# Kernel optimization log

Measured on AMD Instinct MI355X. Metric: run time of the kernel, lower is better.

## Reference

```python
import jax, jax.numpy as jnp
import numpy as np

B = 256        # graphs in batch
N_PER = 512    # nodes per graph (uniform)
D = 256        # in_dim
DEG = 16       # avg degree
RATIO = 0.5


def setup_inputs() -> dict:
    key = jax.random.key(0)
    k1, k2, k3, k4 = jax.random.split(key, 4)
    N = B * N_PER
    e_per = N_PER * DEG
    x = jax.random.normal(k1, (N, D), dtype=jnp.float32)
    # edges confined within each graph (DGL batched-graph structure)
    src = jax.random.randint(k2, (B, e_per), 0, N_PER)
    dst = jax.random.randint(k3, (B, e_per), 0, N_PER)
    offs = jnp.arange(B, dtype=jnp.int32)[:, None] * N_PER
    src = (src + offs).reshape(-1).astype(jnp.int32)
    dst = (dst + offs).reshape(-1).astype(jnp.int32)
    W = jax.random.normal(k4, (D, 1), dtype=jnp.float32) / np.sqrt(D)
    b = jnp.zeros((1,), dtype=jnp.float32)
    num_nodes = jnp.full((B,), N_PER, dtype=jnp.int32)
    return {"x": x, "W": W, "b": b, "src": src, "dst": dst, "num_nodes": num_nodes}


def reference(x, W, b, src, dst, num_nodes):
    N, d = x.shape
    bsz = num_nodes.shape[0]
    n = N // bsz                     # uniform nodes per graph -> static
    k = int(np.ceil(RATIO * n))      # nodes kept per graph (static)

    # ---- GraphConv(in_dim, 1), DGL default norm='both':
    # score = D_in^{-1/2} A D_out^{-1/2} (x W) + b   (W applied first: out_dim < in_dim)
    ones_e = jnp.ones(src.shape, dtype=x.dtype)
    deg_out = jax.ops.segment_sum(ones_e, src, num_segments=N)
    deg_in = jax.ops.segment_sum(ones_e, dst, num_segments=N)
    h = x @ W                                              # [N, 1]
    h = h * jax.lax.rsqrt(jnp.clip(deg_out, 1.0))[:, None]
    agg = jax.ops.segment_sum(h[src], dst, num_segments=N) # [N, 1]
    score = (agg * jax.lax.rsqrt(jnp.clip(deg_in, 1.0))[:, None] + b)[:, 0]  # [N]

    # ---- topk per graph: dense [B, n] buffer is just a reshape (uniform graphs),
    # sort descending + take first k  ==  lax.top_k
    dense = score.reshape(bsz, n)
    _, idx = jax.lax.top_k(dense, k)                       # [B, k] descending
    perm = (idx + jnp.arange(bsz)[:, None] * n).reshape(-1)  # global node ids [B*k]

    # ---- gather + scale: feature[perm] * tanh(score[perm])
    feat = x[perm] * jnp.tanh(score[perm])[:, None]        # [B*k, D]

    # ---- node_subgraph: edges whose both endpoints survive
    keep = jnp.zeros((N,), dtype=bool).at[perm].set(True)
    edge_mask = keep[src] & keep[dst]                      # [E]
    next_num_nodes = jnp.full((bsz,), k, dtype=jnp.int32)
    return feat, perm, edge_mask, next_num_nodes
```

## Files before the change

### kernel.cpp

```cpp
#include <hip/hip_runtime.h>
#include <math.h>

#define BB    256
#define NPER  512
#define DD    256
#define KK    256
#define EPG   (NPER * 16)
#define NN    (BB * NPER)
#define EE    (BB * EPG)

__global__ __launch_bounds__(256) void k_dot(const float* __restrict__ x,
                                             const float* __restrict__ W,
                                             float* __restrict__ hraw) {
    const int wave = threadIdx.x >> 6;
    const int lane = threadIdx.x & 63;
    const int r0   = blockIdx.x * 16 + wave * 4;
    const float4 wv = ((const float4*)W)[lane];
    const float4* p = (const float4*)(x + ((size_t)r0 << 8));
    float4 a0 = p[lane];
    float4 a1 = p[64 + lane];
    float4 a2 = p[128 + lane];
    float4 a3 = p[192 + lane];
    float d0 = a0.x * wv.x + a0.y * wv.y + a0.z * wv.z + a0.w * wv.w;
    float d1 = a1.x * wv.x + a1.y * wv.y + a1.z * wv.z + a1.w * wv.w;
    float d2 = a2.x * wv.x + a2.y * wv.y + a2.z * wv.z + a2.w * wv.w;
    float d3 = a3.x * wv.x + a3.y * wv.y + a3.z * wv.z + a3.w * wv.w;
    #pragma unroll
    for (int off = 32; off > 0; off >>= 1) {
        d0 += __shfl_down(d0, off, 64);
        d1 += __shfl_down(d1, off, 64);
        d2 += __shfl_down(d2, off, 64);
        d3 += __shfl_down(d3, off, 64);
    }
    if (lane == 0) {
        hraw[r0]     = d0;
        hraw[r0 + 1] = d1;
        hraw[r0 + 2] = d2;
        hraw[r0 + 3] = d3;
    }
}

__global__ __launch_bounds__(1024) void k_graph(
        const float* __restrict__ hraw, const float* __restrict__ b,
        const int* __restrict__ src, const int* __restrict__ dst,
        int* __restrict__ perm_i, float* __restrict__ tscore,
        float* __restrict__ out_perm, float* __restrict__ emask,
        float* __restrict__ nnn) {
    __shared__ unsigned short esrc[EPG];
    __shared__ unsigned short edst[EPG];
    __shared__ int   degs[NPER];
    __shared__ int   degd[NPER];
    __shared__ float hl[NPER];
    __shared__ float aggl[NPER];
    __shared__ float scl[NPER];
    __shared__ unsigned long long keys[NPER];
    __shared__ int   keep[NPER];

    const int g = blockIdx.x;
    const int t = threadIdx.x;
    const int nbase = g << 9;

    float hv = 0.0f;
    if (t < NPER) hv = hraw[nbase + t];

    if (t < NPER) { degs[t] = 0; degd[t] = 0; aggl[t] = 0.0f; keep[t] = 0; }
    __syncthreads();

    const int4* s4 = (const int4*)(src + (size_t)g * EPG);
    const int4* d4 = (const int4*)(dst + (size_t)g * EPG);
    unsigned int* es2 = (unsigned int*)esrc;
    unsigned int* ed2 = (unsigned int*)edst;
    #pragma unroll
    for (int i = t; i < EPG / 4; i += 1024) {
        int4 sv = s4[i], dv = d4[i];
        unsigned int s0 = (unsigned int)(sv.x - nbase);
        unsigned int s1 = (unsigned int)(sv.y - nbase);
        unsigned int s2 = (unsigned int)(sv.z - nbase);
        unsigned int s3 = (unsigned int)(sv.w - nbase);
        es2[i * 2]     = s0 | (s1 << 16);
        es2[i * 2 + 1] = s2 | (s3 << 16);
        atomicAdd(&degs[s0], 1); atomicAdd(&degs[s1], 1);
        atomicAdd(&degs[s2], 1); atomicAdd(&degs[s3], 1);
        unsigned int t0 = (unsigned int)(dv.x - nbase);
        unsigned int t1 = (unsigned int)(dv.y - nbase);
        unsigned int t2 = (unsigned int)(dv.z - nbase);
        unsigned int t3 = (unsigned int)(dv.w - nbase);
        ed2[i * 2]     = t0 | (t1 << 16);
        ed2[i * 2 + 1] = t2 | (t3 << 16);
        atomicAdd(&degd[t0], 1); atomicAdd(&degd[t1], 1);
        atomicAdd(&degd[t2], 1); atomicAdd(&degd[t3], 1);
    }
    __syncthreads();

    if (t < NPER) hl[t] = hv * rsqrtf(fmaxf((float)degs[t], 1.0f));
    __syncthreads();

    #pragma unroll
    for (int e = t; e < EPG; e += 1024)
        atomicAdd(&aggl[edst[e]], hl[esrc[e]]);
    __syncthreads();

    if (t < NPER) {
        float sc = aggl[t] * rsqrtf(fmaxf((float)degd[t], 1.0f)) + b[0];
        scl[t] = sc;
        unsigned int u = __float_as_uint(sc);
        u = (u & 0x80000000u) ? ~u : (u | 0x80000000u);
        keys[t] = ((unsigned long long)u << 32) |
                  (unsigned long long)(0xFFFFFFFFu - (unsigned)t);
    }
    __syncthreads();

    for (int kk = 2; kk <= NPER; kk <<= 1) {
        for (int j = kk >> 1; j > 0; j >>= 1) {
            if (t < NPER) {
                int i = t, ixj = t ^ j;
                if (ixj > i) {
                    unsigned long long a = keys[i], c = keys[ixj];
                    bool up = ((i & kk) == 0);
                    if (up ? (a < c) : (a > c)) { keys[i] = c; keys[ixj] = a; }
                }
            }
            __syncthreads();
        }
    }

    if (t < KK) {
        unsigned long long kv = keys[t];
        int idx = (int)(0xFFFFFFFFu - (unsigned int)(kv & 0xFFFFFFFFull));
        int r = (g << 8) + t;
        perm_i[r]   = nbase + idx;
        out_perm[r] = (float)(nbase + idx);
        tscore[r]   = tanhf(scl[idx]);
        keep[idx]   = 1;
    }
    __syncthreads();

    float4* em4 = (float4*)(emask + ((size_t)g << 13));
    #pragma unroll
    for (int i = t; i < EPG / 4; i += 1024) {
        int e = i * 4;
        float4 m;
        m.x = (keep[esrc[e]]     & keep[edst[e]])     ? 1.0f : 0.0f;
        m.y = (keep[esrc[e + 1]] & keep[edst[e + 1]]) ? 1.0f : 0.0f;
        m.z = (keep[esrc[e + 2]] & keep[edst[e + 2]]) ? 1.0f : 0.0f;
        m.w = (keep[esrc[e + 3]] & keep[edst[e + 3]]) ? 1.0f : 0.0f;
        em4[i] = m;
    }
    if (g == 0 && t < BB) nnn[t] = (float)KK;
}

__global__ __launch_bounds__(256) void k_feat(
        const float* __restrict__ x,
        const int* __restrict__ perm_i, const float* __restrict__ tscore,
        float* __restrict__ feat) {
    const int wave = threadIdx.x >> 6;
    const int lane = threadIdx.x & 63;
    const int r = blockIdx.x * 4 + wave;
    const int gid = perm_i[r];
    const float ts = tscore[r];
    float4 v = ((const float4*)(x + ((size_t)gid << 8)))[lane];
    float4 o = make_float4(v.x * ts, v.y * ts, v.z * ts, v.w * ts);
    ((float4*)(feat + ((size_t)r << 8)))[lane] = o;
}

extern "C" void kernel_launch(void* const* d_in, const int* in_sizes, int n_in,
                              void* d_out, int out_size, void* d_ws, size_t ws_size,
                              hipStream_t stream) {
    const float* x   = (const float*)d_in[0];
    const float* W   = (const float*)d_in[1];
    const float* b   = (const float*)d_in[2];
    const int*   src = (const int*)d_in[3];
    const int*   dst = (const int*)d_in[4];

    float* out   = (float*)d_out;
    float* feat  = out;
    float* operm = feat + (size_t)BB * KK * DD;
    float* emask = operm + (size_t)BB * KK;
    float* nnn   = emask + (size_t)EE;

    float* hraw   = (float*)d_ws;
    int*   perm_i = (int*)(hraw + NN);
    float* tscore = (float*)(perm_i + BB * KK);

    k_dot  <<<NN / 16, 256, 0, stream>>>(x, W, hraw);
    k_graph<<<BB, 1024, 0, stream>>>(hraw, b, src, dst, perm_i, tscore,
                                     operm, emask, nnn);
    k_feat <<<BB * KK / 4, 256, 0, stream>>>(x, perm_i, tscore, feat);
}
```

Baseline: 257.6 us.

## Fuse feature gather into graph kernel and use register bitonic sort with shuffles

Merges the separate feature-gather kernel into the per-graph kernel, so the selected indices and tanh scores stay in shared memory and one launch plus a global round-trip of perm/tscore disappear. The bitonic sort now keeps each key in a register and uses wave shuffles for strides below 64, so only large strides touch shared memory and need barriers. Edge loops also read packed 16-bit index pairs, and the keep mask becomes a float multiply. The risk is that the gather now runs on only 256 blocks of 1024 threads, which may reduce parallelism for the feature copy compared with the many small blocks used before.

```diff
diff --git a/kernel.cpp b/kernel.cpp
--- a/kernel.cpp
+++ b/kernel.cpp
@@ -41,54 +41,66 @@
 }
 
 __global__ __launch_bounds__(1024) void k_graph(
+        const float* __restrict__ x,
         const float* __restrict__ hraw, const float* __restrict__ b,
         const int* __restrict__ src, const int* __restrict__ dst,
-        int* __restrict__ perm_i, float* __restrict__ tscore,
-        float* __restrict__ out_perm, float* __restrict__ emask,
-        float* __restrict__ nnn) {
-    __shared__ unsigned short esrc[EPG];
-    __shared__ unsigned short edst[EPG];
+        float* __restrict__ feat, float* __restrict__ out_perm,
+        float* __restrict__ emask, float* __restrict__ nnn) {
+    __shared__ unsigned int es2[EPG / 2];
+    __shared__ unsigned int ed2[EPG / 2];
     __shared__ int   degs[NPER];
     __shared__ int   degd[NPER];
     __shared__ float hl[NPER];
     __shared__ float aggl[NPER];
     __shared__ float scl[NPER];
     __shared__ unsigned long long keys[NPER];
-    __shared__ int   keep[NPER];
+    __shared__ float keepf[NPER];
+    __shared__ int   sel[KK];
+    __shared__ float tsv[KK];
 
     const int g = blockIdx.x;
     const int t = threadIdx.x;
+    const int wave = t >> 6;
+    const int lane = t & 63;
     const int nbase = g << 9;
 
-    float hv = 0.0f;
-    if (t < NPER) hv = hraw[nbase + t];
-
-    if (t < NPER) { degs[t] = 0; degd[t] = 0; aggl[t] = 0.0f; keep[t] = 0; }
+    float hv = (t < NPER) ? hraw[nbase + t] : 0.0f;
+
+    if (t < NPER) { degs[t] = 0; degd[t] = 0; aggl[t] = 0.0f; keepf[t] = 0.0f; }
     __syncthreads();
 
     const int4* s4 = (const int4*)(src + (size_t)g * EPG);
     const int4* d4 = (const int4*)(dst + (size_t)g * EPG);
-    unsigned int* es2 = (unsigned int*)esrc;
-    unsigned int* ed2 = (unsigned int*)edst;
-    #pragma unroll
-    for (int i = t; i < EPG / 4; i += 1024) {
-        int4 sv = s4[i], dv = d4[i];
-        unsigned int s0 = (unsigned int)(sv.x - nbase);
-        unsigned int s1 = (unsigned int)(sv.y - nbase);
-        unsigned int s2 = (unsigned int)(sv.z - nbase);
-        unsigned int s3 = (unsigned int)(sv.w - nbase);
-        es2[i * 2]     = s0 | (s1 << 16);
-        es2[i * 2 + 1] = s2 | (s3 << 16);
-        atomicAdd(&degs[s0], 1); atomicAdd(&degs[s1], 1);
-        atomicAdd(&degs[s2], 1); atomicAdd(&degs[s3], 1);
-        unsigned int t0 = (unsigned int)(dv.x - nbase);
-        unsigned int t1 = (unsigned int)(dv.y - nbase);
-        unsigned int t2 = (unsigned int)(dv.z - nbase);
-        unsigned int t3 = (unsigned int)(dv.w - nbase);
-        ed2[i * 2]     = t0 | (t1 << 16);
-        ed2[i * 2 + 1] = t2 | (t3 << 16);
-        atomicAdd(&degd[t0], 1); atomicAdd(&degd[t1], 1);
-        atomicAdd(&degd[t2], 1); atomicAdd(&degd[t3], 1);
+    int4 sva = s4[t], dva = d4[t];
+    int4 svb = s4[t + 1024], dvb = d4[t + 1024];
+    {
+        unsigned int a0 = (unsigned int)(sva.x - nbase), a1 = (unsigned int)(sva.y - nbase);
+        unsigned int a2 = (unsigned int)(sva.z - nbase), a3 = (unsigned int)(sva.w - nbase);
+        es2[t * 2]     = a0 | (a1 << 16);
+        es2[t * 2 + 1] = a2 | (a3 << 16);
+        atomicAdd(&degs[a0], 1); atomicAdd(&degs[a1], 1);
+        atomicAdd(&degs[a2], 1); atomicAdd(&degs[a3], 1);
+        unsigned int c0 = (unsigned int)(dva.x - nbase), c1 = (unsigned int)(dva.y - nbase);
+        unsigned int c2 = (unsigned int)(dva.z - nbase), c3 = (unsigned int)(dva.w - nbase);
+        ed2[t * 2]     = c0 | (c1 << 16);
+        ed2[t * 2 + 1] = c2 | (c3 << 16);
+        atomicAdd(&degd[c0], 1); atomicAdd(&degd[c1], 1);
+        atomicAdd(&degd[c2], 1); atomicAdd(&degd[c3], 1);
+    }
+    {
+        int i = t + 1024;
+        unsigned int a0 = (unsigned int)(svb.x - nbase), a1 = (unsigned int)(svb.y - nbase);
+        unsigned int a2 = (unsigned int)(svb.z - nbase), a3 = (unsigned int)(svb.w - nbase);
+        es2[i * 2]     = a0 | (a1 << 16);
+        es2[i * 2 + 1] = a2 | (a3 << 16);
+        atomicAdd(&degs[a0], 1); atomicAdd(&degs[a1], 1);
+        atomicAdd(&degs[a2], 1); atomicAdd(&degs[a3], 1);
+        unsigned int c0 = (unsigned int)(dvb.x - nbase), c1 = (unsigned int)(dvb.y - nbase);
+        unsigned int c2 = (unsigned int)(dvb.z - nbase), c3 = (unsigned int)(dvb.w - nbase);
+        ed2[i * 2]     = c0 | (c1 << 16);
+        ed2[i * 2 + 1] = c2 | (c3 << 16);
+        atomicAdd(&degd[c0], 1); atomicAdd(&degd[c1], 1);
+        atomicAdd(&degd[c2], 1); atomicAdd(&degd[c3], 1);
     }
     __syncthreads();
 
@@ -96,71 +108,87 @@
     __syncthreads();
 
     #pragma unroll
-    for (int e = t; e < EPG; e += 1024)
-        atomicAdd(&aggl[edst[e]], hl[esrc[e]]);
-    __syncthreads();
-
+    for (int i = t; i < EPG / 2; i += 1024) {
+        unsigned int sp = es2[i], dp = ed2[i];
+        atomicAdd(&aggl[dp & 0xFFFFu], hl[sp & 0xFFFFu]);
+        atomicAdd(&aggl[dp >> 16],     hl[sp >> 16]);
+    }
+    __syncthreads();
+
+    unsigned long long key = 0;
     if (t < NPER) {
         float sc = aggl[t] * rsqrtf(fmaxf((float)degd[t], 1.0f)) + b[0];
         scl[t] = sc;
         unsigned int u = __float_as_uint(sc);
         u = (u & 0x80000000u) ? ~u : (u | 0x80000000u);
-        keys[t] = ((unsigned long long)u << 32) |
-                  (unsigned long long)(0xFFFFFFFFu - (unsigned)t);
+        key = ((unsigned long long)u << 32) |
+              (unsigned long long)(0xFFFFFFFFu - (unsigned)t);
     }
     __syncthreads();
 
     for (int kk = 2; kk <= NPER; kk <<= 1) {
         for (int j = kk >> 1; j > 0; j >>= 1) {
-            if (t < NPER) {
-                int i = t, ixj = t ^ j;
-                if (ixj > i) {
-                    unsigned long long a = keys[i], c = keys[ixj];
-                    bool up = ((i & kk) == 0);
-                    if (up ? (a < c) : (a > c)) { keys[i] = c; keys[ixj] = a; }
+            if (j >= 64) {
+                __syncthreads();
+                if (t < NPER) keys[t] = key;
+                __syncthreads();
+                if (t < NPER) {
+                    unsigned long long c = keys[t ^ j];
+                    bool lower = ((t & j) == 0);
+                    bool up    = ((t & kk) == 0);
+                    bool takeMax = (up == lower);
+                    key = takeMax ? (key >= c ? key : c)
+                                  : (key >= c ? c : key);
+                }
+            } else {
+                if (t < NPER) {
+                    unsigned long long c = __shfl_xor(key, j, 64);
+                    bool lower = ((t & j) == 0);
+                    bool up    = ((t & kk) == 0);
+                    bool takeMax = (up == lower);
+                    key = takeMax ? (key >= c ? key : c)
+                                  : (key >= c ? c : key);
                 }
             }
-            __syncthreads();
         }
     }
 
     if (t < KK) {
-        unsigned long long kv = keys[t];
-        int idx = (int)(0xFFFFFFFFu - (unsigned int)(kv & 0xFFFFFFFFull));
-        int r = (g << 8) + t;
-        perm_i[r]   = nbase + idx;
-        out_perm[r] = (float)(nbase + idx);
-        tscore[r]   = tanhf(scl[idx]);
-        keep[idx]   = 1;
-    }
-    __syncthreads();
+        int idx = (int)(0xFFFFFFFFu - (unsigned int)(key & 0xFFFFFFFFull));
+        out_perm[(g << 8) + t] = (float)(nbase + idx);
+        sel[t] = idx;
+        tsv[t] = tanhf(scl[idx]);
+        keepf[idx] = 1.0f;
+    }
+    __syncthreads();
+
+    #pragma unroll
+    for (int it = 0; it < 16; it += 2) {
+        const int j0 = wave * 16 + it, j1 = j0 + 1;
+        const int l0 = sel[j0], l1 = sel[j1];
+        const float s0 = tsv[j0], s1 = tsv[j1];
+        const float4* q0 = (const float4*)(x + ((size_t)(nbase + l0) << 8));
+        const float4* q1 = (const float4*)(x + ((size_t)(nbase + l1) << 8));
+        float4 v0 = q0[lane], v1 = q1[lane];
+        float4 o0 = make_float4(v0.x * s0, v0.y * s0, v0.z * s0, v0.w * s0);
+        float4 o1 = make_float4(v1.x * s1, v1.y * s1, v1.z * s1, v1.w * s1);
+        ((float4*)(feat + ((size_t)((g << 8) + j0) << 8)))[lane] = o0;
+        ((float4*)(feat + ((size_t)((g << 8) + j1) << 8)))[lane] = o1;
+    }
 
     float4* em4 = (float4*)(emask + ((size_t)g << 13));
     #pragma unroll
     for (int i = t; i < EPG / 4; i += 1024) {
-        int e = i * 4;
+        unsigned int sp0 = es2[i * 2], sp1 = es2[i * 2 + 1];
+        unsigned int dp0 = ed2[i * 2], dp1 = ed2[i * 2 + 1];
         float4 m;
-        m.x = (keep[esrc[e]]     & keep[edst[e]])     ? 1.0f : 0.0f;
-        m.y = (keep[esrc[e + 1]] & keep[edst[e + 1]]) ? 1.0f : 0.0f;
-        m.z = (keep[esrc[e + 2]] & keep[edst[e + 2]]) ? 1.0f : 0.0f;
-        m.w = (keep[esrc[e + 3]] & keep[edst[e + 3]]) ? 1.0f : 0.0f;
+        m.x = keepf[sp0 & 0xFFFFu] * keepf[dp0 & 0xFFFFu];
+        m.y = keepf[sp0 >> 16]     * keepf[dp0 >> 16];
+        m.z = keepf[sp1 & 0xFFFFu] * keepf[dp1 & 0xFFFFu];
+        m.w = keepf[sp1 >> 16]     * keepf[dp1 >> 16];
         em4[i] = m;
     }
     if (g == 0 && t < BB) nnn[t] = (float)KK;
-}
-
-__global__ __launch_bounds__(256) void k_feat(
-        const float* __restrict__ x,
-        const int* __restrict__ perm_i, const float* __restrict__ tscore,
-        float* __restrict__ feat) {
-    const int wave = threadIdx.x >> 6;
-    const int lane = threadIdx.x & 63;
-    const int r = blockIdx.x * 4 + wave;
-    const int gid = perm_i[r];
-    const float ts = tscore[r];
-    float4 v = ((const float4*)(x + ((size_t)gid << 8)))[lane];
-    float4 o = make_float4(v.x * ts, v.y * ts, v.z * ts, v.w * ts);
-    ((float4*)(feat + ((size_t)r << 8)))[lane] = o;
 }
 
 extern "C" void kernel_launch(void* const* d_in, const int* in_sizes, int n_in,
@@ -178,12 +206,9 @@
     float* emask = operm + (size_t)BB * KK;
     float* nnn   = emask + (size_t)EE;
 
-    float* hraw   = (float*)d_ws;
-    int*   perm_i = (int*)(hraw + NN);
-    float* tscore = (float*)(perm_i + BB * KK);
+    float* hraw = (float*)d_ws;
 
     k_dot  <<<NN / 16, 256, 0, stream>>>(x, W, hraw);
-    k_graph<<<BB, 1024, 0, stream>>>(hraw, b, src, dst, perm_i, tscore,
-                                     operm, emask, nnn);
-    k_feat <<<BB * KK / 4, 256, 0, stream>>>(x, perm_i, tscore, feat);
+    k_graph<<<BB, 1024, 0, stream>>>(x, hraw, b, src, dst,
+                                     feat, operm, emask, nnn);
 }
```

After: 254.6 us. No clear change (-1.2%).
